# Kernel optimization log

Hardware: AMD Instinct MI355X
Metric: run time of the kernel (lower is better)

Reference implementation:

```python
import jax, jax.numpy as jnp
import numpy as np

B, E, H, W, HEADS = 2, 128, 64, 64, 4
FUSED = 2 * E + 1          # concat fusion: C_state + C_trigger + 1 (gnn context)
FC = FUSED // 2            # 128 fusion output channels (= AttentionMIL feature_dim)
EPS = 1e-5
NEG = -1e9


def _conv(x, w, b=None, pad=0):
    out = jax.lax.conv_general_dilated(x, w, (1, 1), [(pad, pad), (pad, pad)],
                                       dimension_numbers=('NCHW', 'OIHW', 'NCHW'))
    return out if b is None else out + b[None, :, None, None]


def _bn(x, g, b):
    # training-mode batchnorm (batch statistics), matching torch default mode
    m = x.mean((0, 2, 3), keepdims=True)
    v = x.var((0, 2, 3), keepdims=True)
    return g[None, :, None, None] * (x - m) * jax.lax.rsqrt(v + EPS) + b[None, :, None, None]


def _mha(q_in, kv_in, w_qkv, b_qkv, w_out, b_out, nheads):
    Bq, L, Em = q_in.shape
    d = Em // nheads
    wq, wk, wv = jnp.split(w_qkv, 3, axis=0)
    bq, bk, bv = jnp.split(b_qkv, 3, axis=0)
    q = (q_in @ wq.T + bq).reshape(Bq, L, nheads, d)
    k = (kv_in @ wk.T + bk).reshape(Bq, -1, nheads, d)
    v = (kv_in @ wv.T + bv).reshape(Bq, -1, nheads, d)
    scores = jnp.einsum('bqhd,bkhd->bhqk', q, k) / jnp.sqrt(jnp.asarray(d, q.dtype))
    attn = jax.nn.softmax(scores, axis=-1)
    out = jnp.einsum('bhqk,bkhd->bqhd', attn, v).reshape(Bq, L, Em)
    return out @ w_out.T + b_out


def setup_inputs() -> dict:
    key = jax.random.key(0)
    ks = jax.random.split(key, 24)
    n = lambda k, s: jax.random.normal(k, s, jnp.float32)
    p = lambda k, s: 0.02 * jax.random.normal(k, s, jnp.float32)
    return dict(
        state_features=n(ks[0], (B, E, H, W)),
        trigger_features=n(ks[1], (B, E, H, W)),
        gnn_context=n(ks[2], (B, 1, H, W)),
        zone_patches=jax.random.randint(ks[3], (B, H, W), 0, 16).astype(jnp.int32),
        cats=jax.random.randint(ks[4], (B,), 0, 16).astype(jnp.int32),
        labels=jax.random.uniform(ks[5], (B,), jnp.float32),
        s2t_qkv_w=p(ks[6], (3 * E, E)), s2t_qkv_b=p(ks[7], (3 * E,)),
        s2t_out_w=p(ks[8], (E, E)), s2t_out_b=p(ks[9], (E,)),
        t2s_qkv_w=p(ks[10], (3 * E, E)), t2s_qkv_b=p(ks[11], (3 * E,)),
        t2s_out_w=p(ks[12], (E, E)), t2s_out_b=p(ks[13], (E,)),
        fconv1_w=p(ks[14], (FC, FUSED, 3, 3)),
        fbn1_g=jnp.ones((FC,), jnp.float32), fbn1_b=jnp.zeros((FC,), jnp.float32),
        fconv2_w=p(ks[15], (FC, FC, 3, 3)),
        fbn2_g=jnp.ones((FC,), jnp.float32), fbn2_b=jnp.zeros((FC,), jnp.float32),
        outc_w=p(ks[16], (1, FC, 1, 1)), outc_b=p(ks[17], (1,)),
        attn1_w=p(ks[18], (128, FC, 1, 1)), attn1_b=p(ks[19], (128,)),
        attn2_w=p(ks[20], (1, 128, 1, 1)), attn2_b=p(ks[21], (1,)),
    )


def reference(state_features, trigger_features, gnn_context, zone_patches, cats, labels,
              s2t_qkv_w, s2t_qkv_b, s2t_out_w, s2t_out_b,
              t2s_qkv_w, t2s_qkv_b, t2s_out_w, t2s_out_b,
              fconv1_w, fbn1_g, fbn1_b, fconv2_w, fbn2_g, fbn2_b,
              outc_w, outc_b, attn1_w, attn1_b, attn2_w, attn2_b):
    Bs = state_features.shape[0]
    # ---- CrossAttentionFusion ----
    sf = state_features.reshape(Bs, E, H * W).transpose(0, 2, 1)    # (B, HW, E)
    tf = trigger_features.reshape(Bs, E, H * W).transpose(0, 2, 1)
    s2t = _mha(sf, tf, s2t_qkv_w, s2t_qkv_b, s2t_out_w, s2t_out_b, HEADS)
    t2s = _mha(tf, sf, t2s_qkv_w, t2s_qkv_b, t2s_out_w, t2s_out_b, HEADS)
    s2t = s2t.transpose(0, 2, 1).reshape(Bs, E, H, W)
    t2s = t2s.transpose(0, 2, 1).reshape(Bs, E, H, W)
    fused = jnp.concatenate([s2t, t2s, gnn_context], axis=1)        # (B, 257, H, W)
    x = jax.nn.relu(_bn(_conv(fused, fconv1_w, pad=1), fbn1_g, fbn1_b))
    feat = jax.nn.relu(_bn(_conv(x, fconv2_w, pad=1), fbn2_g, fbn2_b))  # (B, FC, H, W)
    # ---- pixel logit head (decoder outc) ----
    pixel_logits = _conv(feat, outc_w, outc_b)[:, 0]                # (B, H, W)
    # ---- AttentionMIL (vectorized over batch) ----
    a = jax.nn.relu(_conv(feat, attn1_w, attn1_b))
    scores = _conv(a, attn2_w, attn2_b)[:, 0]                       # (B, H, W)
    mask = (zone_patches == cats[:, None, None]) & (zone_patches > 0)
    has = mask.any((1, 2))
    masked = jnp.where(mask, scores, NEG)                           # score*1 on valid, -1e9 elsewhere
    wts = jax.nn.softmax(masked.reshape(Bs, -1), axis=-1).reshape(Bs, H, W)
    attention_maps = jnp.where(has[:, None, None], wts, 0.0)
    bag = (pixel_logits * wts * mask.astype(wts.dtype)).sum((1, 2))
    bag = jnp.where(has, bag, 0.0)
    # BCEWithLogitsLoss(mean): softplus(x) - x*y
    loss = jnp.mean(jax.nn.softplus(bag) - bag * labels)
    return loss, attention_maps
```

## Files before the change

kernel.cpp:

```cpp
#include <hip/hip_runtime.h>
#include <hip/hip_bf16.h>
#include <math.h>

#define L 4096
#define ECH 128
#define BCH 2
#define NHEAD 4
#define FUSEDC 257
#define CPAD 288

typedef __attribute__((ext_vector_type(8))) short bs8;
typedef __attribute__((ext_vector_type(4))) short bs4;
typedef __attribute__((ext_vector_type(4))) float fx4;

#define SCL 0.25503518f

static __device__ __forceinline__ short f2bfs(float x) {
  unsigned u = __float_as_uint(x);
  u += 0x7fffu + ((u >> 16) & 1u);
  return (short)(u >> 16);
}

static __device__ __forceinline__ float bf2f(short s) {
  return __uint_as_float((unsigned)(unsigned short)s << 16);
}

static __device__ __forceinline__ float exp2a(float x) {
  float r; asm("v_exp_f32 %0, %1" : "=v"(r) : "v"(x)); return r;
}

static __device__ __forceinline__ unsigned pk2(float lo, float hi) {
  unsigned r; asm("v_cvt_pk_bf16_f32 %0, %1, %2" : "=v"(r) : "v"(lo), "v"(hi)); return r;
}

__global__ void prep_fused(const float* __restrict__ c1w, const float* __restrict__ c2w,
                           const float* __restrict__ wS, const float* __restrict__ wT,
                           const float* __restrict__ woS, const float* __restrict__ woT,
                           const float* __restrict__ sf, const float* __restrict__ tf,
                           short* __restrict__ W1b, short* __restrict__ W2b,
                           short* __restrict__ wSb, short* __restrict__ wTb,
                           short* __restrict__ woSb, short* __restrict__ woTb,
                           short* __restrict__ Xs, short* __restrict__ Xt) {
  __shared__ float t[32][33];
  int bid = blockIdx.x;
  if (bid < 2064) {
    int i = bid * 256 + threadIdx.x;
    if (i < 331776) {
      int ci = i % CPAD; int rest = i / CPAD; int co = rest & 127; int tap = rest >> 7;
      W1b[i] = (ci < FUSEDC) ? f2bfs(c1w[(co * FUSEDC + ci) * 9 + tap]) : (short)0;
    } else if (i < 479232) {
      int j = i - 331776;
      int ci = j & 127; int co = (j >> 7) & 127; int tap = j >> 14;
      W2b[j] = f2bfs(c2w[(co * 128 + ci) * 9 + tap]);
    } else {
      int k = i - 479232;
      float s = (k < 16384) ? SCL : 1.0f;
      wSb[k] = f2bfs(wS[k] * s);
      wTb[k] = f2bfs(wT[k] * s);
      if (k < 16384) {
        woSb[k] = f2bfs(woS[k]);
        woTb[k] = f2bfs(woT[k]);
      }
    }
  } else {
    int id = bid - 2064;
    int bx = (id & 127) * 32;
    int by = ((id >> 7) & 3) * 32;
    int z = id >> 9; int b = z & 1; int sel = z >> 1;
    const float* in = sel ? tf : sf;
    short* out = sel ? Xt : Xs;
    int tx = threadIdx.x & 31, ty = threadIdx.x >> 5;
    const float* ip = in + (size_t)b * ECH * L;
    short* op = out + (size_t)b * L * ECH;
#pragma unroll
    for (int r = ty; r < 32; r += 8)
      t[r][tx] = ip[(size_t)(by + r) * L + bx + tx];
    __syncthreads();
#pragma unroll
    for (int r = ty; r < 32; r += 8)
      op[(size_t)(bx + r) * ECH + by + tx] = f2bfs(t[tx][r]);
  }
}

__global__ void __launch_bounds__(256)
gemm_qkv(const short* __restrict__ Xs, const short* __restrict__ Xt,
         const short* __restrict__ wSb, const short* __restrict__ wTb,
         const float* __restrict__ bS, const float* __restrict__ bT,
         short* __restrict__ qs, short* __restrict__ ks,
         short* __restrict__ qt, short* __restrict__ kt,
         short* __restrict__ vTs, short* __restrict__ vTt) {
  int unit = blockIdx.y;
  const short* X; const short* W; const float* bias; short* out; float scale; int mode;
  switch (unit) {
    case 0: X = Xs; W = wSb;         bias = bS;       out = qs;  scale = SCL; mode = 0; break;
    case 1: X = Xt; W = wSb + 16384; bias = bS + 128; out = ks;  scale = 1.f; mode = 1; break;
    case 2: X = Xt; W = wTb;         bias = bT;       out = qt;  scale = SCL; mode = 0; break;
    case 3: X = Xs; W = wTb + 16384; bias = bT + 128; out = kt;  scale = 1.f; mode = 1; break;
    case 4: X = Xt; W = wSb + 32768; bias = bS + 256; out = vTs; scale = 1.f; mode = 2; break;
    default:X = Xs; W = wTb + 32768; bias = bT + 256; out = vTt; scale = 1.f; mode = 2; break;
  }
  int tid = threadIdx.x;
  int wv = tid >> 6, lane = tid & 63, u = lane >> 4, r = lane & 15;
  int pblk = blockIdx.x * 64 + wv * 16;
  const short* xrow = X + (size_t)(pblk + r) * 128;
  fx4 acc[8] = {};
  if (mode != 2) {
#pragma unroll
    for (int ksx = 0; ksx < 4; ++ksx) {
      int k0 = ksx * 32 + u * 8;
      bs8 a = *(const bs8*)(xrow + k0);
      const short* wp = W + (size_t)r * 128 + k0;
#pragma unroll
      for (int t = 0; t < 8; ++t) {
        bs8 wf = *(const bs8*)(wp + (size_t)t * 16 * 128);
        acc[t] = __builtin_amdgcn_mfma_f32_16x16x32_bf16(a, wf, acc[t], 0, 0, 0);
      }
    }
  } else {
#pragma unroll
    for (int ksx = 0; ksx < 4; ++ksx) {
      int k0 = ksx * 32 + u * 8;
      bs8 xb = *(const bs8*)(xrow + k0);
      const short* wp = W + (size_t)r * 128 + k0;
#pragma unroll
      for (int t = 0; t < 8; ++t) {
        bs8 wf = *(const bs8*)(wp + (size_t)t * 16 * 128);
        acc[t] = __builtin_amdgcn_mfma_f32_16x16x32_bf16(wf, xb, acc[t], 0, 0, 0);
      }
    }
  }
  if (mode == 0) {
#pragma unroll
    for (int t = 0; t < 8; ++t) {
      float bv = bias[t * 16 + r] * scale;
#pragma unroll
      for (int reg = 0; reg < 4; ++reg) {
        int p = pblk + u * 4 + reg;
        out[(size_t)p * 128 + t * 16 + r] = f2bfs(acc[t][reg] + bv);
      }
    }
  } else if (mode == 1) {
#pragma unroll
    for (int t = 0; t < 8; ++t) {
      int och = t * 16 + r, h = och >> 5, d = och & 31;
      float bv = bias[och];
#pragma unroll
      for (int reg = 0; reg < 4; ++reg) {
        int p = pblk + u * 4 + reg;
        int b = p >> 12, pl = p & 4095;
        out[(((size_t)(b * NHEAD + h) * L + pl) << 5) + d] = f2bfs(acc[t][reg] + bv);
      }
    }
  } else {
    int p = pblk + r;
    int b = p >> 12, pl = p & 4095;
#pragma unroll
    for (int t = 0; t < 8; ++t) {
#pragma unroll
      for (int reg = 0; reg < 4; ++reg) {
        int och = t * 16 + u * 4 + reg;
        int h = och >> 5, d = och & 31;
        out[((size_t)(b * NHEAD + h) * 32 + d) * L + pl] = f2bfs(acc[t][reg] + bias[och]);
      }
    }
  }
}

__global__ void __launch_bounds__(256)
gemm_o(const short* __restrict__ poS, const float* __restrict__ pmS, const float* __restrict__ plS,
       const short* __restrict__ poT, const float* __restrict__ pmT, const float* __restrict__ plT,
       const short* __restrict__ woSb, const short* __restrict__ woTb,
       const float* __restrict__ boS, const float* __restrict__ boT,
       const float* __restrict__ gnn, short* __restrict__ fusedPM) {
  int unit = blockIdx.y;
  const short* po = unit ? poT : poS;
  const float* pm = unit ? pmT : pmS;
  const float* pl = unit ? plT : plS;
  const short* W = unit ? woTb : woSb;
  const float* bias = unit ? boT : boS;
  int ochbase = unit ? 128 : 0;
  int tid = threadIdx.x;
  int wv = tid >> 6, lane = tid & 63, u = lane >> 4, r = lane & 15;
  int pblk = blockIdx.x * 64 + wv * 16;
  int p = pblk + r, bb = p >> 12, q = p & 4095;
  fx4 acc[8] = {};
#pragma unroll
  for (int ksx = 0; ksx < 4; ++ksx) {
    int row = ((bb * NHEAD + ksx) << 12) + q;
    float m0 = pm[row], m1 = pm[32768 + row];
    float m2 = pm[65536 + row], m3 = pm[98304 + row];
    float l0 = pl[row], l1 = pl[32768 + row];
    float l2 = pl[65536 + row], l3 = pl[98304 + row];
    float mm = fmaxf(fmaxf(m0, m1), fmaxf(m2, m3));
    float f0 = exp2a(m0 - mm), f1 = exp2a(m1 - mm);
    float f2 = exp2a(m2 - mm), f3 = exp2a(m3 - mm);
    float inv = 1.0f / (l0 * f0 + l1 * f1 + l2 * f2 + l3 * f3);
    int base = (row << 5) + u * 8;
    bs8 v0 = *(const bs8*)(po + base);
    bs8 v1 = *(const bs8*)(po + (1 << 20) + base);
    bs8 v2 = *(const bs8*)(po + (2 << 20) + base);
    bs8 v3 = *(const bs8*)(po + (3 << 20) + base);
    union { unsigned w32[4]; bs8 v; } pa;
#pragma unroll
    for (int jj = 0; jj < 4; ++jj) {
      float lo = (bf2f(v0[2 * jj]) * f0 + bf2f(v1[2 * jj]) * f1
                + bf2f(v2[2 * jj]) * f2 + bf2f(v3[2 * jj]) * f3) * inv;
      float hi = (bf2f(v0[2 * jj + 1]) * f0 + bf2f(v1[2 * jj + 1]) * f1
                + bf2f(v2[2 * jj + 1]) * f2 + bf2f(v3[2 * jj + 1]) * f3) * inv;
      pa.w32[jj] = pk2(lo, hi);
    }
    const short* wp = W + (size_t)r * 128 + ksx * 32 + u * 8;
#pragma unroll
    for (int t = 0; t < 8; ++t) {
      bs8 wf = *(const bs8*)(wp + (size_t)t * 16 * 128);
      acc[t] = __builtin_amdgcn_mfma_f32_16x16x32_bf16(pa.v, wf, acc[t], 0, 0, 0);
    }
  }
#pragma unroll
  for (int t = 0; t < 8; ++t) {
    float bv = bias[t * 16 + r];
#pragma unroll
    for (int reg = 0; reg < 4; ++reg) {
      int pp = pblk + u * 4 + reg;
      fusedPM[(size_t)pp * CPAD + ochbase + t * 16 + r] = f2bfs(acc[t][reg] + bv);
    }
  }
  if (unit == 0) {
    int base = blockIdx.x * 64;
    for (int t2 = tid; t2 < 64 * 32; t2 += 256) {
      int pp = base + (t2 >> 5), j = t2 & 31;
      fusedPM[(size_t)pp * CPAD + 256 + j] = (j == 0) ? f2bfs(gnn[pp]) : (short)0;
    }
  }
}

__global__ void __launch_bounds__(256, 4)
flash_attn6(const short* __restrict__ Qs, const short* __restrict__ Ks, const short* __restrict__ Vs,
            const short* __restrict__ Qt, const short* __restrict__ Kt, const short* __restrict__ Vt,
            short* __restrict__ poS, short* __restrict__ poT,
            float* __restrict__ pmS, float* __restrict__ plS,
            float* __restrict__ pmT, float* __restrict__ plT) {
  int z = blockIdx.z;
  int sp = z >> 2, att = (z >> 1) & 1, b = z & 1;
  const short* Q = att ? Qt : Qs;
  const short* K = att ? Kt : Ks;
  const short* VT = att ? Vt : Vs;
  short* po = att ? poT : poS;
  float* pm = att ? pmT : pmS;
  float* pl = att ? plT : plS;
  int tid = threadIdx.x;
  int wid = tid >> 6, lane = tid & 63;
  int u = lane >> 4, r = lane & 15;
  int h = blockIdx.y;
  int qt0 = (blockIdx.x << 4) + (wid << 2);
  bs8 qf0 = *(const bs8*)(Q + ((size_t)(b * L + ((qt0 + 0) << 4) + r) * 128 + h * 32 + u * 8));
  bs8 qf1 = *(const bs8*)(Q + ((size_t)(b * L + ((qt0 + 1) << 4) + r) * 128 + h * 32 + u * 8));
  bs8 qf2 = *(const bs8*)(Q + ((size_t)(b * L + ((qt0 + 2) << 4) + r) * 128 + h * 32 + u * 8));
  bs8 qf3 = *(const bs8*)(Q + ((size_t)(b * L + ((qt0 + 3) << 4) + r) * 128 + h * 32 + u * 8));
  const short* Kb = K + (((size_t)(b * NHEAD + h) * L + sp * 1024) << 5) + u * 8;
  const short* Vb = VT + ((size_t)(b * NHEAD + h) * 32) * (size_t)L + sp * 1024;
  const short* v0p = Vb + (size_t)r * L + (u << 2);
  const short* v1p = Vb + (size_t)(16 + r) * L + (u << 2);
  fx4 o0[4] = {}, o1[4] = {};
  float l[4] = {0.f, 0.f, 0.f, 0.f};
  float m = -1.0e30f;
#pragma unroll 1
  for (int k0 = 0; k0 < 1024; k0 += 64) {
    bs8 a0 = *(const bs8*)(Kb + (((size_t)(k0 + r)) << 5));
    bs8 a1 = *(const bs8*)(Kb + (((size_t)(k0 + 16 + r)) << 5));
    bs8 a2 = *(const bs8*)(Kb + (((size_t)(k0 + 32 + r)) << 5));
    bs8 a3 = *(const bs8*)(Kb + (((size_t)(k0 + 48 + r)) << 5));
    bs4 w0 = *(const bs4*)(v0p + k0);
    bs4 w1 = *(const bs4*)(v0p + k0 + 16);
    bs4 w2 = *(const bs4*)(v0p + k0 + 32);
    bs4 w3 = *(const bs4*)(v0p + k0 + 48);
    bs4 w4 = *(const bs4*)(v1p + k0);
    bs4 w5 = *(const bs4*)(v1p + k0 + 16);
    bs4 w6 = *(const bs4*)(v1p + k0 + 32);
    bs4 w7 = *(const bs4*)(v1p + k0 + 48);
    bs8 vb0lo = __builtin_shufflevector(w0, w1, 0, 1, 2, 3, 4, 5, 6, 7);
    bs8 vb0hi = __builtin_shufflevector(w2, w3, 0, 1, 2, 3, 4, 5, 6, 7);
    bs8 vb1lo = __builtin_shufflevector(w4, w5, 0, 1, 2, 3, 4, 5, 6, 7);
    bs8 vb1hi = __builtin_shufflevector(w6, w7, 0, 1, 2, 3, 4, 5, 6, 7);
    fx4 zz = {0.f, 0.f, 0.f, 0.f};
#pragma unroll
    for (int t = 0; t < 4; ++t) {
      bs8 qf = (t == 0) ? qf0 : (t == 1) ? qf1 : (t == 2) ? qf2 : qf3;
      __builtin_amdgcn_s_setprio(1);
      fx4 s0 = __builtin_amdgcn_mfma_f32_16x16x32_bf16(a0, qf, zz, 0, 0, 0);
      fx4 s1 = __builtin_amdgcn_mfma_f32_16x16x32_bf16(a1, qf, zz, 0, 0, 0);
      fx4 s2 = __builtin_amdgcn_mfma_f32_16x16x32_bf16(a2, qf, zz, 0, 0, 0);
      fx4 s3 = __builtin_amdgcn_mfma_f32_16x16x32_bf16(a3, qf, zz, 0, 0, 0);
      __builtin_amdgcn_s_setprio(0);
      float mx = fmaxf(fmaxf(fmaxf(s0[0], s0[1]), fmaxf(s0[2], s0[3])),
                       fmaxf(fmaxf(s1[0], s1[1]), fmaxf(s1[2], s1[3])));
      mx = fmaxf(mx, fmaxf(fmaxf(fmaxf(s2[0], s2[1]), fmaxf(s2[2], s2[3])),
                           fmaxf(fmaxf(s3[0], s3[1]), fmaxf(s3[2], s3[3]))));
      if (!__all(mx <= m + 8.0f)) {
        float gm = fmaxf(mx, __shfl_xor(mx, 1));
        gm = fmaxf(gm, __shfl_xor(gm, 2));
        gm = fmaxf(gm, __shfl_xor(gm, 4));
        gm = fmaxf(gm, __shfl_xor(gm, 8));
        gm = fmaxf(gm, __shfl_xor(gm, 16));
        gm = fmaxf(gm, __shfl_xor(gm, 32));
        float m_new = fmaxf(m, gm);
        float fsc = exp2a(m - m_new);
#pragma unroll
        for (int tt = 0; tt < 4; ++tt) {
          l[tt] *= fsc;
#pragma unroll
          for (int rg = 0; rg < 4; ++rg) { o0[tt][rg] *= fsc; o1[tt][rg] *= fsc; }
        }
        m = m_new;
      }
      fx4 p0, p1, p2, p3;
#pragma unroll
      for (int i = 0; i < 4; ++i) {
        p0[i] = exp2a(s0[i] - m);
        p1[i] = exp2a(s1[i] - m);
        p2[i] = exp2a(s2[i] - m);
        p3[i] = exp2a(s3[i] - m);
      }
      l[t] += ((p0[0] + p0[1]) + (p0[2] + p0[3])) + ((p1[0] + p1[1]) + (p1[2] + p1[3]))
            + ((p2[0] + p2[1]) + (p2[2] + p2[3])) + ((p3[0] + p3[1]) + (p3[2] + p3[3]));
      union { unsigned w32[4]; bs8 v; } plo, phi;
      plo.w32[0] = pk2(p0[0], p0[1]); plo.w32[1] = pk2(p0[2], p0[3]);
      plo.w32[2] = pk2(p1[0], p1[1]); plo.w32[3] = pk2(p1[2], p1[3]);
      phi.w32[0] = pk2(p2[0], p2[1]); phi.w32[1] = pk2(p2[2], p2[3]);
      phi.w32[2] = pk2(p3[0], p3[1]); phi.w32[3] = pk2(p3[2], p3[3]);
      __builtin_amdgcn_s_setprio(1);
      o0[t] = __builtin_amdgcn_mfma_f32_16x16x32_bf16(plo.v, vb0lo, o0[t], 0, 0, 0);
      o0[t] = __builtin_amdgcn_mfma_f32_16x16x32_bf16(phi.v, vb0hi, o0[t], 0, 0, 0);
      o1[t] = __builtin_amdgcn_mfma_f32_16x16x32_bf16(plo.v, vb1lo, o1[t], 0, 0, 0);
      o1[t] = __builtin_amdgcn_mfma_f32_16x16x32_bf16(phi.v, vb1hi, o1[t], 0, 0, 0);
      __builtin_amdgcn_s_setprio(0);
    }
  }
#pragma unroll
  for (int t = 0; t < 4; ++t) {
    float lt = l[t];
    lt += __shfl_xor(lt, 16);
    lt += __shfl_xor(lt, 32);
    int rowb = ((b * NHEAD + h) << 12) + ((qt0 + t) << 4);
    if (lane < 16) {
      pm[(sp << 15) + rowb + r] = m;
      pl[(sp << 15) + rowb + r] = lt;
    }
#pragma unroll
    for (int reg = 0; reg < 4; ++reg) {
      size_t ob = ((size_t)sp << 20) + ((size_t)(rowb + (u << 2) + reg) << 5);
      po[ob + r] = f2bfs(o0[t][reg]);
      po[ob + 16 + r] = f2bfs(o1[t][reg]);
    }
  }
}

__global__ void __launch_bounds__(128)
conv1_mfma(const short* __restrict__ X, const short* __restrict__ W,
           float* __restrict__ out, float* __restrict__ psum, float* __restrict__ psq) {
  int tid = threadIdx.x;
  int wv = tid >> 6, lane = tid & 63, u = lane >> 4, r = lane & 15;
  int pblk = blockIdx.x * 32 + wv * 16;
  int ybase = blockIdx.y * 32;
  int b = pblk >> 12, y = (pblk & 4095) >> 6, x0 = pblk & 63;
  fx4 acc[2] = {};
  for (int tap = 0; tap < 9; ++tap) {
    int dy = tap / 3 - 1, dx = tap % 3 - 1;
    int yy = y + dy;
    if (yy < 0 || yy > 63) { __syncthreads(); continue; }
    int xx = x0 + r + dx;
    bool valid = (xx >= 0) && (xx <= 63);
    const short* xrow = X + (size_t)((b << 12) + (yy << 6) + x0 + dx + r) * CPAD;
    const short* wtap = W + ((size_t)tap * 128 + ybase + r) * CPAD;
#pragma unroll
    for (int kc = 0; kc < 9; ++kc) {
      int k0 = kc * 32 + u * 8;
      bs8 a = {};
      if (valid) a = *(const bs8*)(xrow + k0);
#pragma unroll
      for (int t = 0; t < 2; ++t) {
        bs8 wf = *(const bs8*)(wtap + (size_t)t * 16 * CPAD + k0);
        acc[t] = __builtin_amdgcn_mfma_f32_16x16x32_bf16(a, wf, acc[t], 0, 0, 0);
      }
    }
    __syncthreads();
  }
#pragma unroll
  for (int t = 0; t < 2; ++t) {
#pragma unroll
    for (int reg = 0; reg < 4; ++reg)
      out[(size_t)(pblk + u * 4 + reg) * 128 + ybase + t * 16 + r] = acc[t][reg];
    float s = (acc[t][0] + acc[t][1]) + (acc[t][2] + acc[t][3]);
    float q = (acc[t][0] * acc[t][0] + acc[t][1] * acc[t][1])
            + (acc[t][2] * acc[t][2] + acc[t][3] * acc[t][3]);
    s += __shfl_xor(s, 16); s += __shfl_xor(s, 32);
    q += __shfl_xor(q, 16); q += __shfl_xor(q, 32);
    if (u == 0) {
      int slot = (ybase + t * 16 + r) * 512 + blockIdx.x * 2 + wv;
      psum[slot] = s;
      psq[slot] = q;
    }
  }
}

__global__ void __launch_bounds__(128)
conv2_mfma(const short* __restrict__ X, const short* __restrict__ W,
           float* __restrict__ out, float* __restrict__ psum, float* __restrict__ psq) {
  int tid = threadIdx.x;
  int wv = tid >> 6, lane = tid & 63, u = lane >> 4, r = lane & 15;
  int pblk = blockIdx.x * 32 + wv * 16;
  int ybase = blockIdx.y * 32;
  int b = pblk >> 12, y = (pblk & 4095) >> 6, x0 = pblk & 63;
  fx4 acc[2] = {};
  for (int tap = 0; tap < 9; ++tap) {
    int dy = tap / 3 - 1, dx = tap % 3 - 1;
    int yy = y + dy;
    if (yy < 0 || yy > 63) { __syncthreads(); continue; }
    int xx = x0 + r + dx;
    bool valid = (xx >= 0) && (xx <= 63);
    const short* xrow = X + (size_t)((b << 12) + (yy << 6) + x0 + dx + r) * 128;
    const short* wtap = W + ((size_t)tap * 128 + ybase + r) * 128;
#pragma unroll
    for (int kc = 0; kc < 4; ++kc) {
      int k0 = kc * 32 + u * 8;
      bs8 xb = {};
      if (valid) xb = *(const bs8*)(xrow + k0);
#pragma unroll
      for (int t = 0; t < 2; ++t) {
        bs8 wf = *(const bs8*)(wtap + (size_t)t * 16 * 128 + k0);
        acc[t] = __builtin_amdgcn_mfma_f32_16x16x32_bf16(wf, xb, acc[t], 0, 0, 0);
      }
    }
    __syncthreads();
  }
  int px = y * 64 + x0 + r;
#pragma unroll
  for (int t = 0; t < 2; ++t) {
#pragma unroll
    for (int reg = 0; reg < 4; ++reg) {
      int och = ybase + t * 16 + u * 4 + reg;
      out[((size_t)(b * 128 + och) << 12) + px] = acc[t][reg];
    }
#pragma unroll
    for (int reg = 0; reg < 4; ++reg) {
      float s = acc[t][reg];
      float q = s * s;
      s += __shfl_xor(s, 1); q += __shfl_xor(q, 1);
      s += __shfl_xor(s, 2); q += __shfl_xor(q, 2);
      s += __shfl_xor(s, 4); q += __shfl_xor(q, 4);
      s += __shfl_xor(s, 8); q += __shfl_xor(q, 8);
      if (r == 0) {
        int slot = (ybase + t * 16 + u * 4 + reg) * 512 + blockIdx.x * 2 + wv;
        psum[slot] = s;
        psq[slot] = q;
      }
    }
  }
}

__global__ void stats_reduce(const float* __restrict__ psum, const float* __restrict__ psq,
                             float* __restrict__ mean, float* __restrict__ rstd) {
  __shared__ float rs[256], rq[256];
  int c = blockIdx.x, tid = threadIdx.x;
  float s = psum[c * 512 + tid] + psum[c * 512 + 256 + tid];
  float q = psq[c * 512 + tid] + psq[c * 512 + 256 + tid];
  rs[tid] = s; rq[tid] = q; __syncthreads();
  for (int st = 128; st > 0; st >>= 1) {
    if (tid < st) { rs[tid] += rs[tid + st]; rq[tid] += rq[tid + st]; }
    __syncthreads();
  }
  if (tid == 0) {
    float m = rs[0] / 8192.0f;
    float v = rq[0] / 8192.0f - m * m;
    mean[c] = m;
    rstd[c] = rsqrtf(v + 1e-5f);
  }
}

__global__ void bnapply_pm(const float* __restrict__ x, const float* __restrict__ mean,
                           const float* __restrict__ rstd, const float* __restrict__ g,
                           const float* __restrict__ bb, short* __restrict__ out) {
  int i = blockIdx.x * 256 + threadIdx.x;
  int c = i & 127;
  float v = x[i];
  out[i] = f2bfs(fmaxf(g[c] * (v - mean[c]) * rstd[c] + bb[c], 0.0f));
}

__global__ void head_kernel(const float* __restrict__ feat,
                            const float* __restrict__ bmean, const float* __restrict__ brstd,
                            const float* __restrict__ bg, const float* __restrict__ bbias,
                            const float* __restrict__ w1, const float* __restrict__ b1,
                            const float* __restrict__ w2, const float* __restrict__ b2,
                            const float* __restrict__ wo, const float* __restrict__ bo,
                            float* __restrict__ score, float* __restrict__ plog) {
  __shared__ float f[128][64];
  __shared__ float r1[4][64], r2[4][64];
  int by = blockIdx.x; int b = by >> 6, y = by & 63;
  int tid = threadIdx.x;
  int x = tid & 63, g4 = tid >> 6;
  for (int c = g4; c < 128; c += 4) {
    float v = feat[((size_t)(b * 128 + c)) * L + y * 64 + x];
    f[c][x] = fmaxf(bg[c] * (v - bmean[c]) * brstd[c] + bbias[c], 0.0f);
  }
  __syncthreads();
  int cb = g4 * 32;
  float a[32];
#pragma unroll
  for (int i = 0; i < 32; ++i) a[i] = b1[cb + i];
  for (int ci = 0; ci < 128; ++ci) {
    float fv = f[ci][x];
#pragma unroll
    for (int i = 0; i < 32; ++i) a[i] += w1[(size_t)(cb + i) * 128 + ci] * fv;
  }
  float sp = 0.0f;
#pragma unroll
  for (int i = 0; i < 32; ++i) sp += w2[cb + i] * fmaxf(a[i], 0.0f);
  float plp = 0.0f;
#pragma unroll
  for (int i = 0; i < 32; ++i) plp += wo[cb + i] * f[cb + i][x];
  r1[g4][x] = sp; r2[g4][x] = plp;
  __syncthreads();
  if (tid < 64) {
    int xx = tid;
    float s = r1[0][xx] + r1[1][xx] + r1[2][xx] + r1[3][xx] + b2[0];
    float pl = r2[0][xx] + r2[1][xx] + r2[2][xx] + r2[3][xx] + bo[0];
    score[(size_t)b * L + y * 64 + xx] = s;
    plog[(size_t)b * L + y * 64 + xx] = pl;
  }
}

__global__ void finalize_kernel(const float* __restrict__ score, const float* __restrict__ plog,
                                const int* __restrict__ zone, const int* __restrict__ cats,
                                float* __restrict__ maps, float* __restrict__ bag_ws) {
  __shared__ float sc[4096];
  __shared__ float red[256];
  __shared__ int ired[256];
  int b = blockIdx.x, tid = threadIdx.x;
  int cat = cats[b];
  float lmax = -3e38f; int lhas = 0;
  for (int p = tid; p < 4096; p += 256) {
    int z = zone[(size_t)b * 4096 + p];
    int m = (z == cat) && (z > 0);
    float s = m ? score[(size_t)b * 4096 + p] : -1e9f;
    sc[p] = s; lmax = fmaxf(lmax, s); lhas |= m;
  }
  red[tid] = lmax; ired[tid] = lhas; __syncthreads();
  for (int st = 128; st > 0; st >>= 1) {
    if (tid < st) { red[tid] = fmaxf(red[tid], red[tid + st]); ired[tid] |= ired[tid + st]; }
    __syncthreads();
  }
  float gmax = red[0]; int has = ired[0];
  __syncthreads();
  float lsum = 0;
  for (int p = tid; p < 4096; p += 256) {
    float e = __expf(sc[p] - gmax);
    sc[p] = e; lsum += e;
  }
  red[tid] = lsum; __syncthreads();
  for (int st = 128; st > 0; st >>= 1) { if (tid < st) red[tid] += red[tid + st]; __syncthreads(); }
  float inv = 1.0f / red[0];
  __syncthreads();
  float lbag = 0;
  for (int p = tid; p < 4096; p += 256) {
    float w = sc[p] * inv;
    maps[(size_t)b * 4096 + p] = has ? w : 0.0f;
    int z = zone[(size_t)b * 4096 + p];
    if ((z == cat) && (z > 0)) lbag += plog[(size_t)b * 4096 + p] * w;
  }
  red[tid] = lbag; __syncthreads();
  for (int st = 128; st > 0; st >>= 1) { if (tid < st) red[tid] += red[tid + st]; __syncthreads(); }
  if (tid == 0) bag_ws[b] = has ? red[0] : 0.0f;
}

__global__ void loss_kernel(const float* __restrict__ bag_ws, const float* __restrict__ labels,
                            float* __restrict__ out) {
  if (threadIdx.x == 0 && blockIdx.x == 0) {
    float t = 0;
    for (int b = 0; b < BCH; ++b) {
      float x = bag_ws[b];
      float sp = fmaxf(x, 0.0f) + log1pf(expf(-fabsf(x)));
      t += sp - x * labels[b];
    }
    out[0] = t / (float)BCH;
  }
}

extern "C" void kernel_launch(void* const* d_in, const int* in_sizes, int n_in,
                              void* d_out, int out_size, void* d_ws, size_t ws_size,
                              hipStream_t stream) {
  (void)in_sizes; (void)n_in; (void)out_size; (void)ws_size;
  const float* state = (const float*)d_in[0];
  const float* trig  = (const float*)d_in[1];
  const float* gnn   = (const float*)d_in[2];
  const int*   zone  = (const int*)d_in[3];
  const int*   cats  = (const int*)d_in[4];
  const float* labels = (const float*)d_in[5];
  const float* s2t_qkv_w = (const float*)d_in[6];
  const float* s2t_qkv_b = (const float*)d_in[7];
  const float* s2t_out_w = (const float*)d_in[8];
  const float* s2t_out_b = (const float*)d_in[9];
  const float* t2s_qkv_w = (const float*)d_in[10];
  const float* t2s_qkv_b = (const float*)d_in[11];
  const float* t2s_out_w = (const float*)d_in[12];
  const float* t2s_out_b = (const float*)d_in[13];
  const float* fconv1_w = (const float*)d_in[14];
  const float* fbn1_g = (const float*)d_in[15];
  const float* fbn1_b = (const float*)d_in[16];
  const float* fconv2_w = (const float*)d_in[17];
  const float* fbn2_g = (const float*)d_in[18];
  const float* fbn2_b = (const float*)d_in[19];
  const float* outc_w = (const float*)d_in[20];
  const float* outc_b = (const float*)d_in[21];
  const float* attn1_w = (const float*)d_in[22];
  const float* attn1_b = (const float*)d_in[23];
  const float* attn2_w = (const float*)d_in[24];
  const float* attn2_b = (const float*)d_in[25];

  float* ws = (float*)d_ws;
  const size_t NBP = (size_t)BCH * L * 128;
  size_t o = 0;
  float* c1 = ws + o; o += NBP;
  float* c2 = ws + o; o += NBP;
  float* stats = ws + o; o += 512;
  float* score = ws + o; o += (size_t)BCH * L;
  float* plog = ws + o; o += (size_t)BCH * L;
  float* bag = ws + o; o += 8;
  short* Xs = (short*)(ws + o); o += NBP / 2;
  short* Xt = (short*)(ws + o); o += NBP / 2;
  short* qsb = (short*)(ws + o); o += NBP / 2;
  short* ksb = (short*)(ws + o); o += NBP / 2;
  short* qtb = (short*)(ws + o); o += NBP / 2;
  short* ktb = (short*)(ws + o); o += NBP / 2;
  short* vTsb = (short*)(ws + o); o += NBP / 2;
  short* vTtb = (short*)(ws + o); o += NBP / 2;
  short* fusedPM = (short*)(ws + o); o += (size_t)BCH * L * CPAD / 2;
  short* X2 = (short*)(ws + o); o += NBP / 2;
  short* W1b = (short*)(ws + o); o += (9 * 128 * CPAD) / 2;
  short* W2b = (short*)(ws + o); o += (9 * 128 * 128) / 2;
  short* wSb = (short*)(ws + o); o += 24576;
  short* wTb = (short*)(ws + o); o += 24576;
  short* woSb = (short*)(ws + o); o += 8192;
  short* woTb = (short*)(ws + o); o += 8192;
  short* poT = (short*)(ws + o); o += 2 * NBP;
  float* psum1 = ws + o; o += 128 * 512;
  float* psq1 = ws + o; o += 128 * 512;
  float* psum2 = ws + o; o += 128 * 512;
  float* psq2 = ws + o; o += 128 * 512;
  float* pmT2 = ws + o; o += 4 * 32768;
  float* plT2 = ws + o; o += 4 * 32768;

  short* poS = (short*)c1;
  float* pmS = (float*)X2;
  float* plS = pmS + 131072;
  float* pmT = pmT2;
  float* plT = plT2;

  prep_fused<<<4112, 256, 0, stream>>>(fconv1_w, fconv2_w, s2t_qkv_w, t2s_qkv_w,
                                       s2t_out_w, t2s_out_w, state, trig,
                                       W1b, W2b, wSb, wTb, woSb, woTb, Xs, Xt);

  gemm_qkv<<<dim3(128, 6), 256, 0, stream>>>(Xs, Xt, wSb, wTb, s2t_qkv_b, t2s_qkv_b,
                                             qsb, ksb, qtb, ktb, vTsb, vTtb);

  flash_attn6<<<dim3(16, NHEAD, 16), 256, 0, stream>>>(qsb, ksb, vTsb, qtb, ktb, vTtb,
                                                       poS, poT, pmS, plS, pmT, plT);

  gemm_o<<<dim3(128, 2), 256, 0, stream>>>(poS, pmS, plS, poT, pmT, plT,
                                           woSb, woTb, s2t_out_b, t2s_out_b,
                                           gnn, fusedPM);

  conv1_mfma<<<dim3(256, 4), 128, 0, stream>>>(fusedPM, W1b, c1, psum1, psq1);
  stats_reduce<<<128, 256, 0, stream>>>(psum1, psq1, stats, stats + 128);
  bnapply_pm<<<4096, 256, 0, stream>>>(c1, stats, stats + 128, fbn1_g, fbn1_b, X2);

  conv2_mfma<<<dim3(256, 4), 128, 0, stream>>>(X2, W2b, c2, psum2, psq2);
  stats_reduce<<<128, 256, 0, stream>>>(psum2, psq2, stats + 256, stats + 384);

  head_kernel<<<BCH * 64, 256, 0, stream>>>(c2, stats + 256, stats + 384, fbn2_g, fbn2_b,
                                            attn1_w, attn1_b, attn2_w, attn2_b,
                                            outc_w, outc_b, score, plog);

  finalize_kernel<<<BCH, 256, 0, stream>>>(score, plog, zone, cats, (float*)d_out + 1, bag);
  loss_kernel<<<1, 64, 0, stream>>>(bag, labels, (float*)d_out);
}
```

Measured before the change: 250.0 us.

## Split flash attention KV range into eight chunks and merge in gemm_o

Doubles the flash-decoding split count from four to eight KV chunks of 512 keys each, giving 2048 blocks instead of 1024, and raises the occupancy hint in launch bounds. gemm_o now merges eight partial outputs with their max and sum statistics. The aim is more parallelism and better latency hiding in the attention stage. In exchange it writes and reads twice as much partial-output traffic, and the extra buffers raise workspace use and register pressure in the merge.

```diff
diff --git a/kernel.cpp b/kernel.cpp
--- a/kernel.cpp
+++ b/kernel.cpp
@@ -167,13 +167,16 @@
 }
 
 __global__ void __launch_bounds__(256)
-gemm_o(const short* __restrict__ poS, const float* __restrict__ pmS, const float* __restrict__ plS,
-       const short* __restrict__ poT, const float* __restrict__ pmT, const float* __restrict__ plT,
+gemm_o(const short* __restrict__ poS0, const short* __restrict__ poS4,
+       const short* __restrict__ poT0, const short* __restrict__ poT4,
+       const float* __restrict__ pmS, const float* __restrict__ plS,
+       const float* __restrict__ pmT, const float* __restrict__ plT,
        const short* __restrict__ woSb, const short* __restrict__ woTb,
        const float* __restrict__ boS, const float* __restrict__ boT,
        const float* __restrict__ gnn, short* __restrict__ fusedPM) {
   int unit = blockIdx.y;
-  const short* po = unit ? poT : poS;
+  const short* p0b = unit ? poT0 : poS0;
+  const short* p4b = unit ? poT4 : poS4;
   const float* pm = unit ? pmT : pmS;
   const float* pl = unit ? plT : plS;
   const short* W = unit ? woTb : woSb;
@@ -187,33 +190,42 @@
 #pragma unroll
   for (int ksx = 0; ksx < 4; ++ksx) {
     int row = ((bb * NHEAD + ksx) << 12) + q;
-    float m0 = pm[row], m1 = pm[32768 + row];
-    float m2 = pm[65536 + row], m3 = pm[98304 + row];
-    float l0 = pl[row], l1 = pl[32768 + row];
-    float l2 = pl[65536 + row], l3 = pl[98304 + row];
-    float mm = fmaxf(fmaxf(m0, m1), fmaxf(m2, m3));
-    float f0 = exp2a(m0 - mm), f1 = exp2a(m1 - mm);
-    float f2 = exp2a(m2 - mm), f3 = exp2a(m3 - mm);
-    float inv = 1.0f / (l0 * f0 + l1 * f1 + l2 * f2 + l3 * f3);
+    float mi[8], li[8];
+#pragma unroll
+    for (int i = 0; i < 8; ++i) {
+      mi[i] = pm[(i << 15) + row];
+      li[i] = pl[(i << 15) + row];
+    }
+    float mm = mi[0];
+#pragma unroll
+    for (int i = 1; i < 8; ++i) mm = fmaxf(mm, mi[i]);
+    float f[8];
+    float den = 0.0f;
+#pragma unroll
+    for (int i = 0; i < 8; ++i) { f[i] = exp2a(mi[i] - mm); den += li[i] * f[i]; }
+    float inv = 1.0f / den;
     int base = (row << 5) + u * 8;
-    bs8 v0 = *(const bs8*)(po + base);
-    bs8 v1 = *(const bs8*)(po + (1 << 20) + base);
-    bs8 v2 = *(const bs8*)(po + (2 << 20) + base);
-    bs8 v3 = *(const bs8*)(po + (3 << 20) + base);
-    union { unsigned w32[4]; bs8 v; } pa;
+    bs8 v[8];
+#pragma unroll
+    for (int i = 0; i < 4; ++i) v[i] = *(const bs8*)(p0b + (((size_t)i) << 20) + base);
+#pragma unroll
+    for (int i = 4; i < 8; ++i) v[i] = *(const bs8*)(p4b + (((size_t)(i - 4)) << 20) + base);
+    union { unsigned w32[4]; bs8 vv; } pa;
 #pragma unroll
     for (int jj = 0; jj < 4; ++jj) {
-      float lo = (bf2f(v0[2 * jj]) * f0 + bf2f(v1[2 * jj]) * f1
-                + bf2f(v2[2 * jj]) * f2 + bf2f(v3[2 * jj]) * f3) * inv;
-      float hi = (bf2f(v0[2 * jj + 1]) * f0 + bf2f(v1[2 * jj + 1]) * f1
-                + bf2f(v2[2 * jj + 1]) * f2 + bf2f(v3[2 * jj + 1]) * f3) * inv;
-      pa.w32[jj] = pk2(lo, hi);
+      float lo = 0.0f, hi = 0.0f;
+#pragma unroll
+      for (int i = 0; i < 8; ++i) {
+        lo += bf2f(v[i][2 * jj]) * f[i];
+        hi += bf2f(v[i][2 * jj + 1]) * f[i];
+      }
+      pa.w32[jj] = pk2(lo * inv, hi * inv);
     }
     const short* wp = W + (size_t)r * 128 + ksx * 32 + u * 8;
 #pragma unroll
     for (int t = 0; t < 8; ++t) {
       bs8 wf = *(const bs8*)(wp + (size_t)t * 16 * 128);
-      acc[t] = __builtin_amdgcn_mfma_f32_16x16x32_bf16(pa.v, wf, acc[t], 0, 0, 0);
+      acc[t] = __builtin_amdgcn_mfma_f32_16x16x32_bf16(pa.vv, wf, acc[t], 0, 0, 0);
     }
   }
 #pragma unroll
@@ -234,10 +246,11 @@
   }
 }
 
-__global__ void __launch_bounds__(256, 4)
+__global__ void __launch_bounds__(256, 8)
 flash_attn6(const short* __restrict__ Qs, const short* __restrict__ Ks, const short* __restrict__ Vs,
             const short* __restrict__ Qt, const short* __restrict__ Kt, const short* __restrict__ Vt,
-            short* __restrict__ poS, short* __restrict__ poT,
+            short* __restrict__ poS0, short* __restrict__ poS4,
+            short* __restrict__ poT0, short* __restrict__ poT4,
             float* __restrict__ pmS, float* __restrict__ plS,
             float* __restrict__ pmT, float* __restrict__ plT) {
   int z = blockIdx.z;
@@ -245,7 +258,10 @@
   const short* Q = att ? Qt : Qs;
   const short* K = att ? Kt : Ks;
   const short* VT = att ? Vt : Vs;
-  short* po = att ? poT : poS;
+  short* base0 = att ? poT0 : poS0;
+  short* base4 = att ? poT4 : poS4;
+  short* po = (sp < 4) ? (base0 + (((size_t)sp) << 20))
+                       : (base4 + (((size_t)(sp - 4)) << 20));
   float* pm = att ? pmT : pmS;
   float* pl = att ? plT : plS;
   int tid = threadIdx.x;
@@ -257,15 +273,15 @@
   bs8 qf1 = *(const bs8*)(Q + ((size_t)(b * L + ((qt0 + 1) << 4) + r) * 128 + h * 32 + u * 8));
   bs8 qf2 = *(const bs8*)(Q + ((size_t)(b * L + ((qt0 + 2) << 4) + r) * 128 + h * 32 + u * 8));
   bs8 qf3 = *(const bs8*)(Q + ((size_t)(b * L + ((qt0 + 3) << 4) + r) * 128 + h * 32 + u * 8));
-  const short* Kb = K + (((size_t)(b * NHEAD + h) * L + sp * 1024) << 5) + u * 8;
-  const short* Vb = VT + ((size_t)(b * NHEAD + h) * 32) * (size_t)L + sp * 1024;
+  const short* Kb = K + (((size_t)(b * NHEAD + h) * L + sp * 512) << 5) + u * 8;
+  const short* Vb = VT + ((size_t)(b * NHEAD + h) * 32) * (size_t)L + sp * 512;
   const short* v0p = Vb + (size_t)r * L + (u << 2);
   const short* v1p = Vb + (size_t)(16 + r) * L + (u << 2);
   fx4 o0[4] = {}, o1[4] = {};
   float l[4] = {0.f, 0.f, 0.f, 0.f};
   float m = -1.0e30f;
 #pragma unroll 1
-  for (int k0 = 0; k0 < 1024; k0 += 64) {
+  for (int k0 = 0; k0 < 512; k0 += 64) {
     bs8 a0 = *(const bs8*)(Kb + (((size_t)(k0 + r)) << 5));
     bs8 a1 = *(const bs8*)(Kb + (((size_t)(k0 + 16 + r)) << 5));
     bs8 a2 = *(const bs8*)(Kb + (((size_t)(k0 + 32 + r)) << 5));
@@ -348,7 +364,7 @@
     }
 #pragma unroll
     for (int reg = 0; reg < 4; ++reg) {
-      size_t ob = ((size_t)sp << 20) + ((size_t)(rowb + (u << 2) + reg) << 5);
+      size_t ob = ((size_t)(rowb + (u << 2) + reg) << 5);
       po[ob + r] = f2bfs(o0[t][reg]);
       po[ob + 16 + r] = f2bfs(o1[t][reg]);
     }
@@ -641,17 +657,19 @@
   short* wTb = (short*)(ws + o); o += 24576;
   short* woSb = (short*)(ws + o); o += 8192;
   short* woTb = (short*)(ws + o); o += 8192;
-  short* poT = (short*)(ws + o); o += 2 * NBP;
+  short* poT0 = (short*)(ws + o); o += 2 * NBP;
+  short* poT4 = (short*)(ws + o); o += 2 * NBP;
+  short* poS4 = (short*)(ws + o); o += 2 * NBP;
   float* psum1 = ws + o; o += 128 * 512;
   float* psq1 = ws + o; o += 128 * 512;
   float* psum2 = ws + o; o += 128 * 512;
   float* psq2 = ws + o; o += 128 * 512;
-  float* pmT2 = ws + o; o += 4 * 32768;
-  float* plT2 = ws + o; o += 4 * 32768;
-
-  short* poS = (short*)c1;
+  float* pmT2 = ws + o; o += 8 * 32768;
+  float* plT2 = ws + o; o += 8 * 32768;
+
+  short* poS0 = (short*)c1;
   float* pmS = (float*)X2;
-  float* plS = pmS + 131072;
+  float* plS = pmS + 8 * 32768;
   float* pmT = pmT2;
   float* plT = plT2;
 
@@ -662,10 +680,12 @@
   gemm_qkv<<<dim3(128, 6), 256, 0, stream>>>(Xs, Xt, wSb, wTb, s2t_qkv_b, t2s_qkv_b,
                                              qsb, ksb, qtb, ktb, vTsb, vTtb);
 
-  flash_attn6<<<dim3(16, NHEAD, 16), 256, 0, stream>>>(qsb, ksb, vTsb, qtb, ktb, vTtb,
-                                                       poS, poT, pmS, plS, pmT, plT);
-
-  gemm_o<<<dim3(128, 2), 256, 0, stream>>>(poS, pmS, plS, poT, pmT, plT,
+  flash_attn6<<<dim3(16, NHEAD, 32), 256, 0, stream>>>(qsb, ksb, vTsb, qtb, ktb, vTtb,
+                                                       poS0, poS4, poT0, poT4,
+                                                       pmS, plS, pmT, plT);
+
+  gemm_o<<<dim3(128, 2), 256, 0, stream>>>(poS0, poS4, poT0, poT4,
+                                           pmS, plS, pmT, plT,
                                            woSb, woTb, s2t_out_b, t2s_out_b,
                                            gnn, fusedPM);
 
```

Result: slower. 676.9 us (+170.8%).
